# Performance work log

Hardware: AMD Instinct MI355X
Metric: run time of the kernel (lower is better)

## Reference

```python
import jax, jax.numpy as jnp
import numpy as np

HEADS = 16
DIM_HEAD = 64
SCALE = DIM_HEAD ** -0.5


def setup_inputs() -> dict:
    key = jax.random.key(0)
    k1, k2, k3 = jax.random.split(key, 3)
    dim, inner = 1024, HEADS * DIM_HEAD
    b, n = 2, 2048
    x = jax.random.normal(k1, (b, n, dim), dtype=jnp.float32)
    w_qkv = jax.random.normal(k2, (dim, 3 * inner), dtype=jnp.float32) * (dim ** -0.5)
    w_out = jax.random.normal(k3, (inner, dim), dtype=jnp.float32) * (inner ** -0.5)
    b_out = jnp.zeros((dim,), dtype=jnp.float32)
    return {"x": x, "w_qkv": w_qkv, "w_out": w_out, "b_out": b_out}


def reference(x, w_qkv, w_out, b_out):
    b, n, _ = x.shape
    qkv = x @ w_qkv                                   # [b,n,3*inner]
    q, k, v = jnp.split(qkv, 3, axis=-1)
    def to_heads(t):
        return t.reshape(b, n, HEADS, DIM_HEAD).transpose(0, 2, 1, 3)  # [b,h,n,d]
    q, k, v = to_heads(q), to_heads(k), to_heads(v)
    dots = jnp.einsum('bhid,bhjd->bhij', q, k) * SCALE  # [b,h,n,n]
    attn = jax.nn.softmax(dots, axis=-1)
    out = jnp.einsum('bhij,bhjd->bhid', attn, v)        # [b,h,n,d]
    out = out.transpose(0, 2, 1, 3).reshape(b, n, HEADS * DIM_HEAD)
    return out @ w_out + b_out
```

## Files before the change

### kernel.cpp

```cpp
#include <hip/hip_runtime.h>
#include <hip/hip_bf16.h>

typedef unsigned short u16;
typedef unsigned int u32;
typedef __attribute__((ext_vector_type(8))) short short8;
typedef __attribute__((ext_vector_type(4))) float f32x4;
typedef __attribute__((ext_vector_type(16))) float f32x16;
typedef __attribute__((ext_vector_type(2))) u32 u32x2;

typedef __attribute__((address_space(1))) void as1_void;
typedef __attribute__((address_space(3))) void as3_void;

__device__ __forceinline__ u16 f2b(float x) {
    union { float f; u32 u; } c; c.f = x;
    u32 r = c.u + 0x7fffu + ((c.u >> 16) & 1u);
    return (u16)(r >> 16);
}
__device__ __forceinline__ float b2f(u16 x) {
    union { u32 u; float f; } c; c.u = ((u32)x) << 16;
    return c.f;
}
__device__ __forceinline__ u32 cvtpk(float lo, float hi) {
    u32 r;
    asm("v_cvt_pk_bf16_f32 %0, %1, %2" : "=v"(r) : "v"(lo), "v"(hi));
    return r;
}
__device__ __forceinline__ void gload16(const u16* g, u16* l) {
    __builtin_amdgcn_global_load_lds((as1_void*)(u16*)g, (as3_void*)l, 16, 0, 0);
}
__device__ __forceinline__ void barrier_raw() {
    asm volatile("" ::: "memory");
    __builtin_amdgcn_s_barrier();
    asm volatile("" ::: "memory");
}

__global__ __launch_bounds__(256) void convert_cvt(const float* __restrict__ in,
                                                   u16* __restrict__ out, int n8) {
    int i = blockIdx.x * 256 + threadIdx.x;
    if (i >= n8) return;
    const float4* p = (const float4*)(in + (size_t)i * 8);
    float4 a = p[0], b = p[1];
    short8 v;
    v[0]=(short)f2b(a.x); v[1]=(short)f2b(a.y); v[2]=(short)f2b(a.z); v[3]=(short)f2b(a.w);
    v[4]=(short)f2b(b.x); v[5]=(short)f2b(b.y); v[6]=(short)f2b(b.z); v[7]=(short)f2b(b.w);
    *(short8*)(out + (size_t)i * 8) = v;
}

__global__ __launch_bounds__(256) void transpose_cvt(const float* __restrict__ in,
                                                     u16* __restrict__ out, int R, int C) {
    __shared__ u16 tile[64][72];
    const int t = threadIdx.x;
    const int r0 = blockIdx.y * 64, c0 = blockIdx.x * 64;
    {
        const int rr = t >> 2;
        const int cq = (t & 3) * 16;
        const float* src = in + (size_t)(r0 + rr) * C + c0 + cq;
        #pragma unroll
        for (int j = 0; j < 4; j++) {
            float4 v = *(const float4*)(src + j * 4);
            tile[cq + j*4 + 0][rr] = f2b(v.x);
            tile[cq + j*4 + 1][rr] = f2b(v.y);
            tile[cq + j*4 + 2][rr] = f2b(v.z);
            tile[cq + j*4 + 3][rr] = f2b(v.w);
        }
    }
    __syncthreads();
    {
        const int cc = t >> 2;
        const int rq = (t & 3) * 16;
        u16* dst = out + (size_t)(c0 + cc) * R + r0 + rq;
        *(short8*)(dst)     = *(const short8*)&tile[cc][rq];
        *(short8*)(dst + 8) = *(const short8*)&tile[cc][rq + 8];
    }
}

template<bool QKV_MODE>
__global__ __launch_bounds__(256) void gemm128(const u16* __restrict__ A,
                                               const u16* __restrict__ Bt,
                                               void* __restrict__ Cp,
                                               u16* __restrict__ vt,
                                               const float* __restrict__ bias,
                                               int M, int Nn, int K) {
    __shared__ __align__(16) u16 a_lds[2][128 * 32];
    __shared__ __align__(16) u16 b_lds[2][128 * 32];
    const int tid = threadIdx.x;
    const int w = tid >> 6, l = tid & 63;
    const int l16 = l & 15, lg = l >> 4;
    const int nbx = gridDim.x;
    const int flat = blockIdx.x + nbx * blockIdx.y;
    const int cpx = (nbx * gridDim.y) >> 3;
    const int logical = (flat & 7) * cpx + (flat >> 3);
    const int m0 = (logical / nbx) * 128, n0 = (logical % nbx) * 128;
    const int wm = w >> 1, wn = w & 1;
    const int lr = l >> 2;
    const int scol = (l & 3) * 8;

    f32x4 acc[4][4];
    #pragma unroll
    for (int i = 0; i < 4; i++)
        #pragma unroll
        for (int j = 0; j < 4; j++) { f32x4 z = {0.f,0.f,0.f,0.f}; acc[i][j] = z; }

    const u16* Ap = A  + (size_t)m0 * K;
    const u16* Bp = Bt + (size_t)n0 * K;

#define STAGE(BUF, KOF)                                                              \
    _Pragma("unroll")                                                                \
    for (int j = 0; j < 2; j++) {                                                    \
        const int r = w * 32 + j * 16;                                               \
        gload16(Ap + (size_t)(r + lr) * K + (KOF) + scol, &a_lds[(BUF)][r * 32]);    \
        gload16(Bp + (size_t)(r + lr) * K + (KOF) + scol, &b_lds[(BUF)][r * 32]);    \
    }

    const int nk = K >> 5;
    STAGE(0, 0)
    int cur = 0;
    for (int kt = 0; kt < nk; kt++) {
        if (kt + 1 < nk) {
            STAGE(cur ^ 1, (kt + 1) << 5)
            __builtin_amdgcn_sched_barrier(0);
            asm volatile("s_waitcnt vmcnt(4)" ::: "memory");
            __builtin_amdgcn_sched_barrier(0);
        } else {
            __builtin_amdgcn_sched_barrier(0);
            asm volatile("s_waitcnt vmcnt(0)" ::: "memory");
            __builtin_amdgcn_sched_barrier(0);
        }
        barrier_raw();
        short8 af[4], bf8[4];
        #pragma unroll
        for (int mb = 0; mb < 4; mb++)
            af[mb] = *(const short8*)&a_lds[cur][(wm * 64 + mb * 16 + l16) * 32 + lg * 8];
        #pragma unroll
        for (int nb = 0; nb < 4; nb++)
            bf8[nb] = *(const short8*)&b_lds[cur][(wn * 64 + nb * 16 + l16) * 32 + lg * 8];
        #pragma unroll
        for (int mb = 0; mb < 4; mb++)
            #pragma unroll
            for (int nb = 0; nb < 4; nb++)
                acc[mb][nb] = __builtin_amdgcn_mfma_f32_16x16x32_bf16(af[mb], bf8[nb], acc[mb][nb], 0, 0, 0);
        barrier_raw();
        cur ^= 1;
    }
#undef STAGE

    #pragma unroll
    for (int mb = 0; mb < 4; mb++) {
        #pragma unroll
        for (int nb = 0; nb < 4; nb++) {
            const int col = n0 + wn * 64 + nb * 16 + l16;
            const int row0 = m0 + wm * 64 + mb * 16 + lg * 4;
            if constexpr (QKV_MODE) {
                if (col < 2048) {
                    #pragma unroll
                    for (int r = 0; r < 4; r++)
                        ((u16*)Cp)[(size_t)(row0 + r) * Nn + col] = f2b(acc[mb][nb][r]);
                } else {
                    const int hd = col - 2048;
                    const int hh = hd >> 6, d = hd & 63;
                    const int bi = row0 >> 11, n = row0 & 2047;
                    u32x2 pr;
                    pr.x = cvtpk(acc[mb][nb][0], acc[mb][nb][1]);
                    pr.y = cvtpk(acc[mb][nb][2], acc[mb][nb][3]);
                    *(u32x2*)(vt + ((size_t)((bi * 16 + hh) * 64 + d)) * 2048 + n) = pr;
                }
            } else {
                #pragma unroll
                for (int r = 0; r < 4; r++)
                    ((float*)Cp)[(size_t)(row0 + r) * Nn + col] = acc[mb][nb][r] + bias[col];
            }
        }
    }
}

__global__ __launch_bounds__(256, 2) void attn_kernel(const u16* __restrict__ qkv,
                                                      const u16* __restrict__ vt,
                                                      u16* __restrict__ out) {
    __shared__ __align__(16) u16 k_lds[8192];
    __shared__ __align__(16) u16 v_lds[8192];
    const int tid = threadIdx.x;
    const int w = tid >> 6, l = tid & 63;
    const int l31 = l & 31, hi = l >> 5;
    const int flat = blockIdx.x + (blockIdx.y << 4) + (blockIdx.z << 8);
    const int logical = (flat & 7) * 64 + (flat >> 3);
    const int xq = logical & 15, h = (logical >> 4) & 15, bb = logical >> 8;
    const int q0 = xq * 128 + w * 32;
    const int swzl = (l31 & 7) << 3;

    const u16* qp = qkv + (size_t)(bb * 2048 + q0 + l31) * 3072 + h * 64 + hi * 8;
    short8 qf[4];
    #pragma unroll
    for (int c4 = 0; c4 < 4; c4++) {
        short8 v = *(const short8*)(qp + c4 * 16);
        #pragma unroll
        for (int e = 0; e < 8; e++) v[e] = (short)f2b(b2f((u16)v[e]) * 0.125f);
        qf[c4] = v;
    }

    f32x16 o[2];
    #pragma unroll
    for (int d0 = 0; d0 < 2; d0++)
        #pragma unroll
        for (int e = 0; e < 16; e++) o[d0][e] = 0.f;
    float mrow = -1e30f, lsum = 0.f;

    const int srow = tid >> 2, sc = tid & 3;
    const int kd0 = srow * 64 + ((sc ^ (srow & 7)) * 8);
    const int kd1 = srow * 64 + (((sc + 4) ^ (srow & 7)) * 8);
    const u16* ksrc = qkv + (size_t)(bb * 2048 + srow) * 3072 + 1024 + h * 64 + sc * 8;
    const u16* vsrc = vt + (size_t)((bb * 16 + h) * 64 + srow) * 2048 + sc * 8;

    short8 kr0 = *(const short8*)ksrc, kr1 = *(const short8*)(ksrc + 32);
    short8 vr0 = *(const short8*)vsrc, vr1 = *(const short8*)(vsrc + 32);
    ksrc += 64 * 3072; vsrc += 64;
    *(short8*)&k_lds[kd0] = kr0; *(short8*)&k_lds[kd1] = kr1;
    *(short8*)&v_lds[kd0] = vr0; *(short8*)&v_lds[kd1] = vr1;
    __syncthreads();

#define DO_TILE(CUR, NXT)                                                               \
  {                                                                                     \
     \
    kr0 = *(const short8*)ksrc; kr1 = *(const short8*)(ksrc + 32);                      \
    vr0 = *(const short8*)vsrc; vr1 = *(const short8*)(vsrc + 32);                      \
    ksrc += 64 * 3072; vsrc += 64;                                                      \
    f32x16 st[2];                                                                       \
    _Pragma("unroll") for (int tt = 0; tt < 2; tt++)                                    \
      _Pragma("unroll") for (int e = 0; e < 16; e++) st[tt][e] = 0.f;                   \
    _Pragma("unroll")                                                                   \
    for (int c4 = 0; c4 < 4; c4++) {                                                    \
      short8 kf0 = *(const short8*)&k_lds[(CUR) + (l31)*64      + ((c4*16 + hi*8) ^ swzl)]; \
      short8 kf1 = *(const short8*)&k_lds[(CUR) + (32 + l31)*64 + ((c4*16 + hi*8) ^ swzl)]; \
      st[0] = __builtin_amdgcn_mfma_f32_32x32x16_bf16(kf0, qf[c4], st[0], 0, 0, 0);     \
      st[1] = __builtin_amdgcn_mfma_f32_32x32x16_bf16(kf1, qf[c4], st[1], 0, 0, 0);     \
    }                                                                                   \
    float pmax = st[0][0];                                                              \
    _Pragma("unroll") for (int e = 1; e < 16; e++) pmax = fmaxf(pmax, st[0][e]);        \
    _Pragma("unroll") for (int e = 0; e < 16; e++) pmax = fmaxf(pmax, st[1][e]);        \
    const float rowm = fmaxf(pmax, __shfl_xor(pmax, 32));                               \
    if (__any(rowm > mrow + 5.5451774f)) {              \
      const float mnew  = fmaxf(mrow, rowm);                                            \
      const float alpha = __expf(mrow - mnew);                                          \
      lsum *= alpha;                                                                    \
      _Pragma("unroll") for (int d0 = 0; d0 < 2; d0++)                                  \
        _Pragma("unroll") for (int e = 0; e < 16; e++) o[d0][e] *= alpha;               \
      mrow = mnew;                                                                      \
    }                                                                                   \
    _Pragma("unroll") for (int tt = 0; tt < 2; tt++)                                    \
      _Pragma("unroll") for (int e = 0; e < 16; e++) st[tt][e] = __expf(st[tt][e] - mrow); \
    float psum = 0.f;                                                                   \
    _Pragma("unroll") for (int tt = 0; tt < 2; tt++)                                    \
      _Pragma("unroll") for (int e = 0; e < 16; e++) psum += st[tt][e];                 \
    lsum += psum + __shfl_xor(psum, 32);                                                \
    short8 pb[4];                                                                       \
    _Pragma("unroll")                                                                   \
    for (int tt = 0; tt < 2; tt++) {                                                    \
      _Pragma("unroll")                                                                 \
      for (int g = 0; g < 2; g++) {                                                     \
         \
        u32 w0 = cvtpk(st[tt][8*g + 0], st[tt][8*g + 1]);                               \
        u32 w1 = cvtpk(st[tt][8*g + 2], st[tt][8*g + 3]);                               \
        u32 w2 = cvtpk(st[tt][8*g + 4], st[tt][8*g + 5]);                               \
        u32 w3 = cvtpk(st[tt][8*g + 6], st[tt][8*g + 7]);                               \
        u32 w0x = (u32)__shfl_xor((int)w0, 32);                                         \
        u32 w1x = (u32)__shfl_xor((int)w1, 32);                                         \
        u32 w2x = (u32)__shfl_xor((int)w2, 32);                                         \
        u32 w3x = (u32)__shfl_xor((int)w3, 32);                                         \
        union { u32 wd[4]; short8 s8; } uu;                                             \
        uu.wd[0] = hi ? w2x : w0;                                                       \
        uu.wd[1] = hi ? w3x : w1;                                                       \
        uu.wd[2] = hi ? w2  : w0x;                                                      \
        uu.wd[3] = hi ? w3  : w1x;                                                      \
        pb[2*tt + g] = uu.s8;                                                           \
      }                                                                                 \
    }                                                                                   \
    _Pragma("unroll")                                                                   \
    for (int ks = 0; ks < 4; ks++) {                                                    \
      short8 vf0 = *(const short8*)&v_lds[(CUR) + (l31)*64      + ((ks*16 + hi*8) ^ swzl)]; \
      short8 vf1 = *(const short8*)&v_lds[(CUR) + (32 + l31)*64 + ((ks*16 + hi*8) ^ swzl)]; \
      o[0] = __builtin_amdgcn_mfma_f32_32x32x16_bf16(vf0, pb[ks], o[0], 0, 0, 0);       \
      o[1] = __builtin_amdgcn_mfma_f32_32x32x16_bf16(vf1, pb[ks], o[1], 0, 0, 0);       \
    }                                                                                   \
    *(short8*)&k_lds[(NXT) + kd0] = kr0; *(short8*)&k_lds[(NXT) + kd1] = kr1;           \
    *(short8*)&v_lds[(NXT) + kd0] = vr0; *(short8*)&v_lds[(NXT) + kd1] = vr1;           \
    __syncthreads();                                                                    \
  }

    for (int it = 0; it < 16; it++) {
        DO_TILE(0, 4096)
        DO_TILE(4096, 0)
    }
#undef DO_TILE

    const float invl = 1.0f / lsum;
    u16* op = out + (size_t)(bb * 2048 + q0 + l31) * 1024 + h * 64;
    #pragma unroll
    for (int d0 = 0; d0 < 2; d0++) {
        #pragma unroll
        for (int s = 0; s < 4; s++) {
            u32x2 pr;
            pr.x = cvtpk(o[d0][4*s + 0] * invl, o[d0][4*s + 1] * invl);
            pr.y = cvtpk(o[d0][4*s + 2] * invl, o[d0][4*s + 3] * invl);
            *(u32x2*)(op + d0 * 32 + s * 8 + hi * 4) = pr;
        }
    }
}

extern "C" void kernel_launch(void* const* d_in, const int* in_sizes, int n_in,
                              void* d_out, int out_size, void* d_ws, size_t ws_size,
                              hipStream_t stream) {
    const float* x     = (const float*)d_in[0];
    const float* w_qkv = (const float*)d_in[1];
    const float* w_out = (const float*)d_in[2];
    const float* b_out = (const float*)d_in[3];

    char* ws = (char*)d_ws;
    u16* xb    = (u16*)(ws);
    u16* wqkvT = (u16*)(ws + (size_t)( 8u << 20));
    u16* woutT = (u16*)(ws + (size_t)(14u << 20));
    u16* qkvb  = (u16*)(ws + (size_t)(16u << 20));
    u16* vtb   = (u16*)(ws + (size_t)(40u << 20));
    u16* aout  = (u16*)(ws + (size_t)(48u << 20));

    convert_cvt<<<2048, 256, 0, stream>>>(x, xb, 4096 * 1024 / 8);
    transpose_cvt<<<dim3(48, 16), 256, 0, stream>>>(w_qkv, wqkvT, 1024, 3072);
    transpose_cvt<<<dim3(16, 16), 256, 0, stream>>>(w_out, woutT, 1024, 1024);

    gemm128<true><<<dim3(24, 32), 256, 0, stream>>>(xb, wqkvT, qkvb, vtb, nullptr,
                                                    4096, 3072, 1024);
    attn_kernel<<<dim3(16, 16, 2), 256, 0, stream>>>(qkvb, vtb, aout);

    gemm128<false><<<dim3(8, 32), 256, 0, stream>>>(aout, woutT, d_out, nullptr, b_out,
                                                    4096, 1024, 1024);
}
```

Measured before the change: 127.6 us.

## Split attention KV range across two wave groups and merge partial softmax

The attention block grows to 512 threads. Two groups of four waves each process half of the key/value sequence for the same 128 queries, with separate double-buffered LDS regions. At the end the second group writes its partial output, max and sum to LDS, and the first group merges them with rescaling before storing. This halves the serial KV loop per block and raises waves per CU, at the cost of more LDS (64KB per block), an extra merge step, and more register pressure under the launch bounds.

```diff
diff --git a/kernel.cpp b/kernel.cpp
--- a/kernel.cpp
+++ b/kernel.cpp
@@ -173,18 +173,20 @@
     }
 }
 
-__global__ __launch_bounds__(256, 2) void attn_kernel(const u16* __restrict__ qkv,
+__global__ __launch_bounds__(512, 2) void attn_kernel(const u16* __restrict__ qkv,
                                                       const u16* __restrict__ vt,
                                                       u16* __restrict__ out) {
-    __shared__ __align__(16) u16 k_lds[8192];
-    __shared__ __align__(16) u16 v_lds[8192];
+    __shared__ __align__(16) u16 lds[32768];
     const int tid = threadIdx.x;
     const int w = tid >> 6, l = tid & 63;
+    const int kvh = w >> 2, wq = w & 3;
     const int l31 = l & 31, hi = l >> 5;
     const int flat = blockIdx.x + (blockIdx.y << 4) + (blockIdx.z << 8);
     const int logical = (flat & 7) * 64 + (flat >> 3);
     const int xq = logical & 15, h = (logical >> 4) & 15, bb = logical >> 8;
-    const int q0 = xq * 128 + w * 32;
+    const int q0 = xq * 128 + wq * 32;
+    const int base_k = kvh * 8192;
+    const int base_v = 16384 + kvh * 8192;
     const int swzl = (l31 & 7) << 3;
 
     const u16* qp = qkv + (size_t)(bb * 2048 + q0 + l31) * 3072 + h * 64 + hi * 8;
@@ -204,17 +206,18 @@
         for (int e = 0; e < 16; e++) o[d0][e] = 0.f;
     float mrow = -1e30f, lsum = 0.f;
 
-    const int srow = tid >> 2, sc = tid & 3;
+    const int t256 = tid & 255;
+    const int srow = t256 >> 2, sc = t256 & 3;
     const int kd0 = srow * 64 + ((sc ^ (srow & 7)) * 8);
     const int kd1 = srow * 64 + (((sc + 4) ^ (srow & 7)) * 8);
-    const u16* ksrc = qkv + (size_t)(bb * 2048 + srow) * 3072 + 1024 + h * 64 + sc * 8;
-    const u16* vsrc = vt + (size_t)((bb * 16 + h) * 64 + srow) * 2048 + sc * 8;
+    const u16* ksrc = qkv + (size_t)(bb * 2048 + kvh * 1024 + srow) * 3072 + 1024 + h * 64 + sc * 8;
+    const u16* vsrc = vt + (size_t)((bb * 16 + h) * 64 + srow) * 2048 + kvh * 1024 + sc * 8;
 
     short8 kr0 = *(const short8*)ksrc, kr1 = *(const short8*)(ksrc + 32);
     short8 vr0 = *(const short8*)vsrc, vr1 = *(const short8*)(vsrc + 32);
     ksrc += 64 * 3072; vsrc += 64;
-    *(short8*)&k_lds[kd0] = kr0; *(short8*)&k_lds[kd1] = kr1;
-    *(short8*)&v_lds[kd0] = vr0; *(short8*)&v_lds[kd1] = vr1;
+    *(short8*)&lds[base_k + kd0] = kr0; *(short8*)&lds[base_k + kd1] = kr1;
+    *(short8*)&lds[base_v + kd0] = vr0; *(short8*)&lds[base_v + kd1] = vr1;
     __syncthreads();
 
 #define DO_TILE(CUR, NXT)                                                               \
@@ -228,8 +231,8 @@
       _Pragma("unroll") for (int e = 0; e < 16; e++) st[tt][e] = 0.f;                   \
     _Pragma("unroll")                                                                   \
     for (int c4 = 0; c4 < 4; c4++) {                                                    \
-      short8 kf0 = *(const short8*)&k_lds[(CUR) + (l31)*64      + ((c4*16 + hi*8) ^ swzl)]; \
-      short8 kf1 = *(const short8*)&k_lds[(CUR) + (32 + l31)*64 + ((c4*16 + hi*8) ^ swzl)]; \
+      short8 kf0 = *(const short8*)&lds[base_k + (CUR) + (l31)*64      + ((c4*16 + hi*8) ^ swzl)]; \
+      short8 kf1 = *(const short8*)&lds[base_k + (CUR) + (32 + l31)*64 + ((c4*16 + hi*8) ^ swzl)]; \
       st[0] = __builtin_amdgcn_mfma_f32_32x32x16_bf16(kf0, qf[c4], st[0], 0, 0, 0);     \
       st[1] = __builtin_amdgcn_mfma_f32_32x32x16_bf16(kf1, qf[c4], st[1], 0, 0, 0);     \
     }                                                                                   \
@@ -275,32 +278,50 @@
     }                                                                                   \
     _Pragma("unroll")                                                                   \
     for (int ks = 0; ks < 4; ks++) {                                                    \
-      short8 vf0 = *(const short8*)&v_lds[(CUR) + (l31)*64      + ((ks*16 + hi*8) ^ swzl)]; \
-      short8 vf1 = *(const short8*)&v_lds[(CUR) + (32 + l31)*64 + ((ks*16 + hi*8) ^ swzl)]; \
+      short8 vf0 = *(const short8*)&lds[base_v + (CUR) + (l31)*64      + ((ks*16 + hi*8) ^ swzl)]; \
+      short8 vf1 = *(const short8*)&lds[base_v + (CUR) + (32 + l31)*64 + ((ks*16 + hi*8) ^ swzl)]; \
       o[0] = __builtin_amdgcn_mfma_f32_32x32x16_bf16(vf0, pb[ks], o[0], 0, 0, 0);       \
       o[1] = __builtin_amdgcn_mfma_f32_32x32x16_bf16(vf1, pb[ks], o[1], 0, 0, 0);       \
     }                                                                                   \
-    *(short8*)&k_lds[(NXT) + kd0] = kr0; *(short8*)&k_lds[(NXT) + kd1] = kr1;           \
-    *(short8*)&v_lds[(NXT) + kd0] = vr0; *(short8*)&v_lds[(NXT) + kd1] = vr1;           \
+    *(short8*)&lds[base_k + (NXT) + kd0] = kr0; *(short8*)&lds[base_k + (NXT) + kd1] = kr1; \
+    *(short8*)&lds[base_v + (NXT) + kd0] = vr0; *(short8*)&lds[base_v + (NXT) + kd1] = vr1; \
     __syncthreads();                                                                    \
   }
 
-    for (int it = 0; it < 16; it++) {
+    for (int it = 0; it < 8; it++) {
         DO_TILE(0, 4096)
         DO_TILE(4096, 0)
     }
 #undef DO_TILE
 
-    const float invl = 1.0f / lsum;
-    u16* op = out + (size_t)(bb * 2048 + q0 + l31) * 1024 + h * 64;
-    #pragma unroll
-    for (int d0 = 0; d0 < 2; d0++) {
-        #pragma unroll
-        for (int s = 0; s < 4; s++) {
-            u32x2 pr;
-            pr.x = cvtpk(o[d0][4*s + 0] * invl, o[d0][4*s + 1] * invl);
-            pr.y = cvtpk(o[d0][4*s + 2] * invl, o[d0][4*s + 3] * invl);
-            *(u32x2*)(op + d0 * 32 + s * 8 + hi * 4) = pr;
+    __syncthreads();
+    float* fl = (float*)lds;
+    float* slot = fl + (wq * 64 + l) * 36;
+    if (kvh) {
+        #pragma unroll
+        for (int d0 = 0; d0 < 2; d0++)
+            #pragma unroll
+            for (int e = 0; e < 16; e++) slot[d0 * 16 + e] = o[d0][e];
+        slot[32] = mrow; slot[33] = lsum;
+    }
+    __syncthreads();
+    if (!kvh) {
+        const float m1 = slot[32], l1v = slot[33];
+        const float m = fmaxf(mrow, m1);
+        const float a0 = __expf(mrow - m), a1 = __expf(m1 - m);
+        const float invl = 1.0f / (lsum * a0 + l1v * a1);
+        u16* op = out + (size_t)(bb * 2048 + q0 + l31) * 1024 + h * 64;
+        #pragma unroll
+        for (int d0 = 0; d0 < 2; d0++) {
+            #pragma unroll
+            for (int s = 0; s < 4; s++) {
+                float c0 = (o[d0][4*s + 0] * a0 + slot[d0*16 + 4*s + 0] * a1) * invl;
+                float c1 = (o[d0][4*s + 1] * a0 + slot[d0*16 + 4*s + 1] * a1) * invl;
+                float c2 = (o[d0][4*s + 2] * a0 + slot[d0*16 + 4*s + 2] * a1) * invl;
+                float c3 = (o[d0][4*s + 3] * a0 + slot[d0*16 + 4*s + 3] * a1) * invl;
+                u32x2 pr; pr.x = cvtpk(c0, c1); pr.y = cvtpk(c2, c3);
+                *(u32x2*)(op + d0 * 32 + s * 8 + hi * 4) = pr;
+            }
         }
     }
 }
@@ -327,7 +348,7 @@
 
     gemm128<true><<<dim3(24, 32), 256, 0, stream>>>(xb, wqkvT, qkvb, vtb, nullptr,
                                                     4096, 3072, 1024);
-    attn_kernel<<<dim3(16, 16, 2), 256, 0, stream>>>(qkvb, vtb, aout);
+    attn_kernel<<<dim3(16, 16, 2), 512, 0, stream>>>(qkvb, vtb, aout);
 
     gemm128<false><<<dim3(8, 32), 256, 0, stream>>>(aout, woutT, d_out, nullptr, b_out,
                                                     4096, 1024, 1024);
```

New measurement: 131.6 us. 3.2% more time.
